# Kernel tuning notes

Measured on AMD Instinct MI355X. Metric: run time of the kernel, lower is better.

## Reference

```python
import jax, jax.numpy as jnp
import numpy as np

V_MIN = -10.0
V_MAX = 10.0
NUM_ATOMS = 251
B = 131072
N_OBS = 128
N_ACT = 32
HID = 512


def _ln(x, g, b, eps=1e-5):
    m = jnp.mean(x, axis=-1, keepdims=True)
    v = jnp.var(x, axis=-1, keepdims=True)
    return (x - m) * jax.lax.rsqrt(v + eps) * g + b


def setup_inputs() -> dict:
    key = jax.random.key(0)
    ks = jax.random.split(key, 16)

    def lin(k, fi, fo):
        kw, kb = jax.random.split(k)
        lim = 1.0 / np.sqrt(fi)
        W = jax.random.uniform(kw, (fi, fo), jnp.float32, -lim, lim)
        b = jax.random.uniform(kb, (fo,), jnp.float32, -lim, lim)
        return W, b

    W1, b1 = lin(ks[0], N_OBS + N_ACT, HID)
    W2, b2 = lin(ks[1], HID, HID // 2)
    W3, b3 = lin(ks[2], HID // 2, HID // 4)
    W4, b4 = lin(ks[3], HID // 4, NUM_ATOMS)

    return {
        "obs": jax.random.normal(ks[4], (B, N_OBS), jnp.float32),
        "actions": jax.random.normal(ks[5], (B, N_ACT), jnp.float32),
        "rewards": jax.random.normal(ks[6], (B,), jnp.float32),
        "bootstrap": (jax.random.uniform(ks[7], (B,)) > 0.05).astype(jnp.float32),
        "discount": jnp.full((B,), 0.99, jnp.float32),
        "q_support": jnp.linspace(V_MIN, V_MAX, NUM_ATOMS, dtype=jnp.float32),
        "W1": W1, "b1": b1, "g1": jnp.ones((HID,), jnp.float32), "be1": jnp.zeros((HID,), jnp.float32),
        "W2": W2, "b2": b2, "g2": jnp.ones((HID // 2,), jnp.float32), "be2": jnp.zeros((HID // 2,), jnp.float32),
        "W3": W3, "b3": b3, "g3": jnp.ones((HID // 4,), jnp.float32), "be3": jnp.zeros((HID // 4,), jnp.float32),
        "W4": W4, "b4": b4,
    }


def _net(obs, actions, W1, b1, g1, be1, W2, b2, g2, be2, W3, b3, g3, be3, W4, b4):
    x = jnp.concatenate([obs, actions], axis=1)
    x = jax.nn.silu(_ln(x @ W1 + b1, g1, be1))
    x = jax.nn.silu(_ln(x @ W2 + b2, g2, be2))
    x = jax.nn.silu(_ln(x @ W3 + b3, g3, be3))
    return x @ W4 + b4  # [B, NUM_ATOMS] logits


def reference(obs, actions, rewards, bootstrap, discount, q_support,
              W1, b1, g1, be1, W2, b2, g2, be2, W3, b3, g3, be3, W4, b4):
    # C51 categorical projection (DistributionalQNetwork.projection)
    delta_z = (V_MAX - V_MIN) / (NUM_ATOMS - 1)
    bsz = rewards.shape[0]
    target_z = rewards[:, None] + bootstrap[:, None] * discount[:, None] * q_support[None, :]
    target_z = jnp.clip(target_z, V_MIN, V_MAX)
    b = (target_z - V_MIN) / delta_z  # fractional bin positions [B, A]
    lower = jnp.floor(b).astype(jnp.int32)
    upper = jnp.ceil(b).astype(jnp.int32)
    is_integer = upper == lower
    lower_mask = (lower > 0) & is_integer
    upper_mask = (lower == 0) & is_integer
    lower = jnp.where(lower_mask, lower - 1, lower)
    upper = jnp.where(upper_mask, upper + 1, upper)

    logits = _net(obs, actions, W1, b1, g1, be1, W2, b2, g2, be2, W3, b3, g3, be3, W4, b4)
    next_dist = jax.nn.softmax(logits, axis=1)

    offset = (jnp.arange(bsz, dtype=jnp.int32) * NUM_ATOMS)[:, None]  # [B,1]
    max_index = bsz * NUM_ATOMS - 1
    li = jnp.clip((lower + offset).reshape(-1), 0, max_index)
    ui = jnp.clip((upper + offset).reshape(-1), 0, max_index)

    w_lo = (next_dist * (upper.astype(jnp.float32) - b)).reshape(-1)
    w_hi = (next_dist * (b - lower.astype(jnp.float32))).reshape(-1)

    proj = jnp.zeros((bsz * NUM_ATOMS,), next_dist.dtype)
    proj = proj.at[li].add(w_lo).at[ui].add(w_hi)
    return proj.reshape(bsz, NUM_ATOMS)
```

## Files before the change

kernel.cpp:

```cpp
#include <hip/hip_runtime.h>


#define THREADS 256
#define PREP_THREADS 256

typedef __attribute__((ext_vector_type(8))) short short8v;
typedef __attribute__((ext_vector_type(4))) float f32x4;

__device__ __forceinline__ unsigned short f2bf(float f) {
  union { float f; unsigned u; } v; v.f = f;
  unsigned u = v.u;
  u += 0x7fffu + ((u >> 16) & 1u);
  return (unsigned short)(u >> 16);
}
__device__ __forceinline__ unsigned pack2bf(float a, float b) {
  return (unsigned)f2bf(a) | ((unsigned)f2bf(b) << 16);
}

__global__ void prep_kernel(const float* __restrict__ W1, const float* __restrict__ W2,
                            const float* __restrict__ W3, const float* __restrict__ W4,
                            unsigned short* __restrict__ ws) {
  int i = blockIdx.x * PREP_THREADS + threadIdx.x;
  if (i < 81920) {
    int n = i / 160, k = i - n * 160;
    ws[i] = f2bf(W1[k * 512 + n]);
  } else if (i < 212992) {
    int j = i - 81920; int n = j >> 9, k = j & 511;
    ws[i] = f2bf(W2[k * 256 + n]);
  } else if (i < 245760) {
    int j = i - 212992; int n = j >> 8, k = j & 255;
    ws[i] = f2bf(W3[k * 128 + n]);
  } else if (i < 278528) {
    int j = i - 245760; int n = j >> 7, k = j & 127;
    ws[i] = (n < 251) ? f2bf(W4[k * 251 + n]) : (unsigned short)0;
  }
}

#define OFF_R   0
#define OFF_ZS  32768
#define OFF_B4  33792
#define OFF_RED 34816
#define LDS_TOTAL 36096

template<int KD, int NFT>
__device__ __forceinline__ void gemm_w(const unsigned short* __restrict__ WT,
                                       const unsigned char* __restrict__ Hb,
                                       int fbase, f32x4 (&acc)[NFT][2]) {
  const int lane = threadIdx.x & 63;
  const int lm = lane & 15, kg = lane >> 4;
  constexpr int KS  = KD / 32;
  constexpr int G   = (NFT > 4) ? 2 : 1;
  constexpr int FPG = NFT / G;
  constexpr int NIT = KS * G;

  int woff[NFT];
#pragma unroll
  for (int ft = 0; ft < NFT; ++ft)
    woff[ft] = (fbase + ft * 16 + lm) * KD + kg * 8;

  int boff[2][2];
#pragma unroll
  for (int rt = 0; rt < 2; ++rt) {
    const int r = rt * 16 + lm;
    const int swz = (r & 7) << 4;
    const int base = r * (KD * 2) + kg * 16;
    boff[rt][0] = base ^ swz;
    boff[rt][1] = (base + 64) ^ swz;
  }

  short8v abuf[2][FPG];
  short8v bbuf[2][2];
#pragma unroll
  for (int rt = 0; rt < 2; ++rt)
    bbuf[0][rt] = *(const short8v*)(Hb + boff[rt][0]);
#pragma unroll
  for (int f = 0; f < FPG; ++f)
    abuf[0][f] = *(const short8v*)(WT + woff[f]);

#pragma unroll
  for (int it = 0; it < NIT; ++it) {
    const int ks = it / G, g = it % G;
    const int cur = it & 1, nxt = cur ^ 1;
    if (it + 1 < NIT) {
      const int nit = it + 1;
      const int nks = nit / G, ng = nit % G;
      if (ng == 0) {
        const int koff = (nks >> 1) * 128;
#pragma unroll
        for (int rt = 0; rt < 2; ++rt)
          bbuf[nks & 1][rt] = *(const short8v*)(Hb + boff[rt][nks & 1] + koff);
      }
#pragma unroll
      for (int f = 0; f < FPG; ++f)
        abuf[nxt][f] = *(const short8v*)(WT + woff[ng * FPG + f] + nks * 32);
    }
#pragma unroll
    for (int f = 0; f < FPG; ++f) {
      const int ft = g * FPG + f;
      acc[ft][0] = __builtin_amdgcn_mfma_f32_16x16x32_bf16(abuf[cur][f], bbuf[ks & 1][0], acc[ft][0], 0, 0, 0);
      acc[ft][1] = __builtin_amdgcn_mfma_f32_16x16x32_bf16(abuf[cur][f], bbuf[ks & 1][1], acc[ft][1], 0, 0, 0);
    }
  }
}

template<int ND, int NFT>
__device__ __forceinline__ void ln_silu_store(
    f32x4 (&acc)[NFT][2],
    const float* __restrict__ bias, const float* __restrict__ g,
    const float* __restrict__ be, unsigned char* __restrict__ Hb,
    float* __restrict__ redL, int fbase, int fq)
{
  const int lane = threadIdx.x & 63;
  const int lm = lane & 15, kg = lane >> 4;
  float s[2] = {0.f, 0.f}, q[2] = {0.f, 0.f};
#pragma unroll
  for (int ft = 0; ft < NFT; ++ft) {
    const int f0 = fbase + ft * 16 + kg * 4;
    const f32x4 bb = *(const f32x4*)(bias + f0);
#pragma unroll
    for (int rt = 0; rt < 2; ++rt)
#pragma unroll
      for (int rg = 0; rg < 4; ++rg) {
        float x = acc[ft][rt][rg] + bb[rg];
        acc[ft][rt][rg] = x;
        s[rt] += x; q[rt] += x * x;
      }
  }
#pragma unroll
  for (int rt = 0; rt < 2; ++rt) {
    s[rt] += __shfl_xor(s[rt], 16); s[rt] += __shfl_xor(s[rt], 32);
    q[rt] += __shfl_xor(q[rt], 16); q[rt] += __shfl_xor(q[rt], 32);
  }
  if (lane < 16) {
#pragma unroll
    for (int rt = 0; rt < 2; ++rt) {
      redL[(rt * 16 + lm) * 9 + fq * 2    ] = s[rt];
      redL[(rt * 16 + lm) * 9 + fq * 2 + 1] = q[rt];
    }
  }
  __syncthreads();
  float mean[2], rstd[2];
#pragma unroll
  for (int rt = 0; rt < 2; ++rt) {
    const int row = rt * 16 + lm;
    float S = 0.f, Q = 0.f;
#pragma unroll
    for (int w = 0; w < 4; ++w) {
      S += redL[row * 9 + w * 2];
      Q += redL[row * 9 + w * 2 + 1];
    }
    float m = S * (1.0f / ND);
    float v = Q * (1.0f / ND) - m * m;
    mean[rt] = m; rstd[rt] = rsqrtf(v + 1e-5f);
  }
#pragma unroll
  for (int ft = 0; ft < NFT; ++ft) {
    const int f0 = fbase + ft * 16 + kg * 4;
    const f32x4 g4 = *(const f32x4*)(g + f0);
    const f32x4 e4 = *(const f32x4*)(be + f0);
#pragma unroll
    for (int rt = 0; rt < 2; ++rt) {
      const int row = rt * 16 + lm;
      float h[4];
#pragma unroll
      for (int rg = 0; rg < 4; ++rg) {
        float y = (acc[ft][rt][rg] - mean[rt]) * rstd[rt] * g4[rg] + e4[rg];
        h[rg] = y * (1.0f / (1.0f + __expf(-y)));
      }
      uint2 w; w.x = pack2bf(h[0], h[1]); w.y = pack2bf(h[2], h[3]);
      int byte = row * (ND * 2) + f0 * 2;
      byte ^= ((row & 7) << 4);
      *(uint2*)(Hb + byte) = w;
    }
  }
}

__global__ __launch_bounds__(THREADS, 4) void fused_kernel(
    const float* __restrict__ obs, const float* __restrict__ actions,
    const float* __restrict__ rewards, const float* __restrict__ bootstrap,
    const float* __restrict__ discount, const float* __restrict__ q_support,
    const float* __restrict__ b1, const float* __restrict__ g1, const float* __restrict__ be1,
    const float* __restrict__ b2, const float* __restrict__ g2, const float* __restrict__ be2,
    const float* __restrict__ b3, const float* __restrict__ g3, const float* __restrict__ be3,
    const float* __restrict__ b4,
    const unsigned short* __restrict__ ws,
    float* __restrict__ out)
{
  __shared__ __align__(16) unsigned char smem[LDS_TOTAL];
  const int tid  = threadIdx.x;
  const int fq   = tid >> 6;
  const int lane = tid & 63;
  const int lm   = lane & 15;
  const int kg   = lane >> 4;
  const int row0 = blockIdx.x * 32;

  const unsigned short* W1T = ws;
  const unsigned short* W2T = ws + 81920;
  const unsigned short* W3T = ws + 212992;
  const unsigned short* W4T = ws + 245760;

  float* zsL  = (float*)(smem + OFF_ZS);
  float* b4L  = (float*)(smem + OFF_B4);
  float* redL = (float*)(smem + OFF_RED);

  float rw[2], bt[2], dc[2];
#pragma unroll
  for (int rt = 0; rt < 2; ++rt) {
    const int r = row0 + rt * 16 + lm;
    rw[rt] = rewards[r]; bt[rt] = bootstrap[r]; dc[rt] = discount[r];
  }

  zsL[tid] = (tid < 251) ? q_support[tid] : 0.f;
  b4L[tid] = (tid < 251) ? b4[tid] : 0.f;

  {
    unsigned char* Xb = smem + OFF_R;
#pragma unroll
    for (int it = 0; it < 5; ++it) {
      const int qq = it * THREADS + tid;
      const int r  = qq / 40;
      const int c4 = (qq - r * 40) * 4;
      float4 v;
      if (c4 < 128) v = *(const float4*)(obs + (size_t)(row0 + r) * 128 + c4);
      else          v = *(const float4*)(actions + (size_t)(row0 + r) * 32 + (c4 - 128));
      uint2 w; w.x = pack2bf(v.x, v.y); w.y = pack2bf(v.z, v.w);
      int byte = r * 320 + c4 * 2;
      byte ^= ((r & 7) << 4);
      *(uint2*)(Xb + byte) = w;
    }
  }
  __syncthreads();

  f32x4 acc1[8][2];
#pragma unroll
  for (int i = 0; i < 8; ++i) { acc1[i][0] = f32x4{0,0,0,0}; acc1[i][1] = f32x4{0,0,0,0}; }
  gemm_w<160, 8>(W1T, smem + OFF_R, fq * 128, acc1);
  ln_silu_store<512, 8>(acc1, b1, g1, be1, smem + OFF_R, redL, fq * 128, fq);
  __syncthreads();

  f32x4 acc2[4][2];
#pragma unroll
  for (int i = 0; i < 4; ++i) { acc2[i][0] = f32x4{0,0,0,0}; acc2[i][1] = f32x4{0,0,0,0}; }
  gemm_w<512, 4>(W2T, smem + OFF_R, fq * 64, acc2);
  ln_silu_store<256, 4>(acc2, b2, g2, be2, smem + OFF_R, redL, fq * 64, fq);
  __syncthreads();

  f32x4 acc3[2][2];
#pragma unroll
  for (int i = 0; i < 2; ++i) { acc3[i][0] = f32x4{0,0,0,0}; acc3[i][1] = f32x4{0,0,0,0}; }
  gemm_w<256, 2>(W3T, smem + OFF_R, fq * 32, acc3);
  ln_silu_store<128, 2>(acc3, b3, g3, be3, smem + OFF_R, redL, fq * 32, fq);
  __syncthreads();

  f32x4 acc4[4][2];
#pragma unroll
  for (int i = 0; i < 4; ++i) { acc4[i][0] = f32x4{0,0,0,0}; acc4[i][1] = f32x4{0,0,0,0}; }
  gemm_w<128, 4>(W4T, smem + OFF_R, fq * 64, acc4);

  float lv[4][2][4];
#pragma unroll
  for (int ft = 0; ft < 4; ++ft) {
    const int f0 = fq * 64 + ft * 16 + kg * 4;
    const f32x4 bb = *(const f32x4*)(b4L + f0);
#pragma unroll
    for (int rt = 0; rt < 2; ++rt)
#pragma unroll
      for (int rg = 0; rg < 4; ++rg) {
        const int f = f0 + rg;
        lv[ft][rt][rg] = (f < 251) ? (acc4[ft][rt][rg] + bb[rg]) : -1e30f;
      }
  }

#pragma unroll
  for (int rt = 0; rt < 2; ++rt) {
    float m = lv[0][rt][0];
#pragma unroll
    for (int ft = 0; ft < 4; ++ft)
#pragma unroll
      for (int rg = 0; rg < 4; ++rg) m = fmaxf(m, lv[ft][rt][rg]);
    m = fmaxf(m, __shfl_xor(m, 16));
    m = fmaxf(m, __shfl_xor(m, 32));
    if (lane < 16) redL[(rt * 16 + lm) * 5 + fq] = m;
  }
  __syncthreads();

  float* projL = (float*)(smem + OFF_R);
  for (int i = tid; i < 32 * 251; i += THREADS) projL[i] = 0.f;

  float gm[2];
#pragma unroll
  for (int rt = 0; rt < 2; ++rt) {
    const int row = rt * 16 + lm;
    float m = redL[row * 5];
#pragma unroll
    for (int w = 1; w < 4; ++w) m = fmaxf(m, redL[row * 5 + w]);
    gm[rt] = m;
  }
  __syncthreads();
#pragma unroll
  for (int rt = 0; rt < 2; ++rt) {
    float E = 0.f;
#pragma unroll
    for (int ft = 0; ft < 4; ++ft)
#pragma unroll
      for (int rg = 0; rg < 4; ++rg) {
        float e = __expf(lv[ft][rt][rg] - gm[rt]);
        lv[ft][rt][rg] = e;
        E += e;
      }
    E += __shfl_xor(E, 16); E += __shfl_xor(E, 32);
    if (lane < 16) redL[(rt * 16 + lm) * 5 + fq] = E;
  }
  __syncthreads();
  float inv[2];
#pragma unroll
  for (int rt = 0; rt < 2; ++rt) {
    const int row = rt * 16 + lm;
    float E = 0.f;
#pragma unroll
    for (int w = 0; w < 4; ++w) E += redL[row * 5 + w];
    inv[rt] = 1.0f / E;
  }

  constexpr float DZF = 20.0f / 250.0f;
#pragma unroll
  for (int ft = 0; ft < 4; ++ft) {
    const int f0 = fq * 64 + ft * 16 + kg * 4;
    const f32x4 z4 = *(const f32x4*)(zsL + f0);
#pragma unroll
    for (int rt = 0; rt < 2; ++rt) {
      const int base = (rt * 16 + lm) * 251;
      const float bd = __fmul_rn(bt[rt], dc[rt]);
#pragma unroll
      for (int rg = 0; rg < 4; ++rg) {
        const int f = f0 + rg;
        if (f < 251) {
          const float p = lv[ft][rt][rg] * inv[rt];
          float t = __fadd_rn(rw[rt], __fmul_rn(bd, z4[rg]));
          t = fminf(fmaxf(t, -10.0f), 10.0f);
          const float bfr = __fdiv_rn(__fsub_rn(t, -10.0f), DZF);
          const float fl = floorf(bfr), fu = ceilf(bfr);
          int l = (int)fl, u = (int)fu;
          if (fl == fu) { if (l > 0) --l; else ++u; }
          atomicAdd(projL + base + l, p * ((float)u - bfr));
          atomicAdd(projL + base + u, p * (bfr - (float)l));
        }
      }
    }
  }
  __syncthreads();

  const float4* ps = (const float4*)projL;
  float4* po = (float4*)(out + (size_t)row0 * 251);
  for (int i = tid; i < 2008; i += THREADS) po[i] = ps[i];
}

extern "C" void kernel_launch(void* const* d_in, const int* in_sizes, int n_in,
                              void* d_out, int out_size, void* d_ws, size_t ws_size,
                              hipStream_t stream) {
  const float* obs  = (const float*)d_in[0];
  const float* act  = (const float*)d_in[1];
  const float* rew  = (const float*)d_in[2];
  const float* boot = (const float*)d_in[3];
  const float* disc = (const float*)d_in[4];
  const float* zs   = (const float*)d_in[5];
  const float* W1   = (const float*)d_in[6];
  const float* b1   = (const float*)d_in[7];
  const float* g1   = (const float*)d_in[8];
  const float* be1  = (const float*)d_in[9];
  const float* W2   = (const float*)d_in[10];
  const float* b2   = (const float*)d_in[11];
  const float* g2   = (const float*)d_in[12];
  const float* be2  = (const float*)d_in[13];
  const float* W3   = (const float*)d_in[14];
  const float* b3   = (const float*)d_in[15];
  const float* g3   = (const float*)d_in[16];
  const float* be3  = (const float*)d_in[17];
  const float* W4   = (const float*)d_in[18];
  const float* b4   = (const float*)d_in[19];
  unsigned short* wsp = (unsigned short*)d_ws;

  const int Bn = in_sizes[2];
  prep_kernel<<<(278528 + PREP_THREADS - 1) / PREP_THREADS, PREP_THREADS, 0, stream>>>(
      W1, W2, W3, W4, wsp);
  fused_kernel<<<Bn / 32, THREADS, 0, stream>>>(obs, act, rew, boot, disc, zs,
      b1, g1, be1, b2, g2, be2, b3, g3, be3, b4, wsp, (float*)d_out);
}
```

Baseline: 482.8 us.

## Halve rows per block to 16 and use hardware bf16 pack instruction

Each block now handles 16 batch rows instead of 32, so every MFMA uses one B tile rather than two. This halves accumulator registers and LDS, and the launch bound rises to 6 blocks per SM for higher occupancy. It also replaces the software bf16 rounding in pack2bf with the v_cvt_pk_bf16_f32 instruction. The cost is that each weight fragment loaded from global or L2 is reused across half as many rows, which doubles weight traffic per row.

```diff
diff --git a/kernel.cpp b/kernel.cpp
--- a/kernel.cpp
+++ b/kernel.cpp
@@ -14,7 +14,9 @@
   return (unsigned short)(u >> 16);
 }
 __device__ __forceinline__ unsigned pack2bf(float a, float b) {
-  return (unsigned)f2bf(a) | ((unsigned)f2bf(b) << 16);
+  unsigned r;
+  asm("v_cvt_pk_bf16_f32 %0, %1, %2" : "=v"(r) : "v"(a), "v"(b));
+  return r;
 }
 
 __global__ void prep_kernel(const float* __restrict__ W1, const float* __restrict__ W2,
@@ -37,15 +39,15 @@
 }
 
 #define OFF_R   0
-#define OFF_ZS  32768
-#define OFF_B4  33792
-#define OFF_RED 34816
-#define LDS_TOTAL 36096
+#define OFF_ZS  16384
+#define OFF_B4  17408
+#define OFF_RED 18432
+#define LDS_TOTAL 19008
 
 template<int KD, int NFT>
 __device__ __forceinline__ void gemm_w(const unsigned short* __restrict__ WT,
                                        const unsigned char* __restrict__ Hb,
-                                       int fbase, f32x4 (&acc)[NFT][2]) {
+                                       int fbase, f32x4 (&acc)[NFT]) {
   const int lane = threadIdx.x & 63;
   const int lm = lane & 15, kg = lane >> 4;
   constexpr int KS  = KD / 32;
@@ -53,29 +55,19 @@
   constexpr int FPG = NFT / G;
   constexpr int NIT = KS * G;
 
-  int woff[NFT];
-#pragma unroll
-  for (int ft = 0; ft < NFT; ++ft)
-    woff[ft] = (fbase + ft * 16 + lm) * KD + kg * 8;
-
-  int boff[2][2];
-#pragma unroll
-  for (int rt = 0; rt < 2; ++rt) {
-    const int r = rt * 16 + lm;
-    const int swz = (r & 7) << 4;
-    const int base = r * (KD * 2) + kg * 16;
-    boff[rt][0] = base ^ swz;
-    boff[rt][1] = (base + 64) ^ swz;
-  }
+  const int woff0 = (fbase + lm) * KD + kg * 8;
+  const int r = lm;
+  const int swz = (r & 7) << 4;
+  const int bbase = r * (KD * 2) + kg * 16;
+  const int boff0 = bbase ^ swz;
+  const int boff1 = (bbase + 64) ^ swz;
 
   short8v abuf[2][FPG];
-  short8v bbuf[2][2];
-#pragma unroll
-  for (int rt = 0; rt < 2; ++rt)
-    bbuf[0][rt] = *(const short8v*)(Hb + boff[rt][0]);
+  short8v bbuf[2];
+  bbuf[0] = *(const short8v*)(Hb + boff0);
 #pragma unroll
   for (int f = 0; f < FPG; ++f)
-    abuf[0][f] = *(const short8v*)(WT + woff[f]);
+    abuf[0][f] = *(const short8v*)(WT + woff0 + f * (16 * KD));
 
 #pragma unroll
   for (int it = 0; it < NIT; ++it) {
@@ -86,96 +78,76 @@
       const int nks = nit / G, ng = nit % G;
       if (ng == 0) {
         const int koff = (nks >> 1) * 128;
-#pragma unroll
-        for (int rt = 0; rt < 2; ++rt)
-          bbuf[nks & 1][rt] = *(const short8v*)(Hb + boff[rt][nks & 1] + koff);
+        bbuf[nks & 1] = *(const short8v*)(Hb + ((nks & 1) ? boff1 : boff0) + koff);
       }
 #pragma unroll
       for (int f = 0; f < FPG; ++f)
-        abuf[nxt][f] = *(const short8v*)(WT + woff[ng * FPG + f] + nks * 32);
+        abuf[nxt][f] = *(const short8v*)(WT + woff0 + (ng * FPG + f) * (16 * KD) + nks * 32);
     }
 #pragma unroll
     for (int f = 0; f < FPG; ++f) {
       const int ft = g * FPG + f;
-      acc[ft][0] = __builtin_amdgcn_mfma_f32_16x16x32_bf16(abuf[cur][f], bbuf[ks & 1][0], acc[ft][0], 0, 0, 0);
-      acc[ft][1] = __builtin_amdgcn_mfma_f32_16x16x32_bf16(abuf[cur][f], bbuf[ks & 1][1], acc[ft][1], 0, 0, 0);
+      acc[ft] = __builtin_amdgcn_mfma_f32_16x16x32_bf16(abuf[cur][f], bbuf[ks & 1], acc[ft], 0, 0, 0);
     }
   }
 }
 
 template<int ND, int NFT>
 __device__ __forceinline__ void ln_silu_store(
-    f32x4 (&acc)[NFT][2],
+    f32x4 (&acc)[NFT],
     const float* __restrict__ bias, const float* __restrict__ g,
     const float* __restrict__ be, unsigned char* __restrict__ Hb,
     float* __restrict__ redL, int fbase, int fq)
 {
   const int lane = threadIdx.x & 63;
   const int lm = lane & 15, kg = lane >> 4;
-  float s[2] = {0.f, 0.f}, q[2] = {0.f, 0.f};
+  float s = 0.f, q = 0.f;
 #pragma unroll
   for (int ft = 0; ft < NFT; ++ft) {
     const int f0 = fbase + ft * 16 + kg * 4;
     const f32x4 bb = *(const f32x4*)(bias + f0);
 #pragma unroll
-    for (int rt = 0; rt < 2; ++rt)
-#pragma unroll
-      for (int rg = 0; rg < 4; ++rg) {
-        float x = acc[ft][rt][rg] + bb[rg];
-        acc[ft][rt][rg] = x;
-        s[rt] += x; q[rt] += x * x;
-      }
-  }
-#pragma unroll
-  for (int rt = 0; rt < 2; ++rt) {
-    s[rt] += __shfl_xor(s[rt], 16); s[rt] += __shfl_xor(s[rt], 32);
-    q[rt] += __shfl_xor(q[rt], 16); q[rt] += __shfl_xor(q[rt], 32);
-  }
+    for (int rg = 0; rg < 4; ++rg) {
+      float x = acc[ft][rg] + bb[rg];
+      acc[ft][rg] = x;
+      s += x; q += x * x;
+    }
+  }
+  s += __shfl_xor(s, 16); s += __shfl_xor(s, 32);
+  q += __shfl_xor(q, 16); q += __shfl_xor(q, 32);
   if (lane < 16) {
-#pragma unroll
-    for (int rt = 0; rt < 2; ++rt) {
-      redL[(rt * 16 + lm) * 9 + fq * 2    ] = s[rt];
-      redL[(rt * 16 + lm) * 9 + fq * 2 + 1] = q[rt];
-    }
-  }
-  __syncthreads();
-  float mean[2], rstd[2];
-#pragma unroll
-  for (int rt = 0; rt < 2; ++rt) {
-    const int row = rt * 16 + lm;
-    float S = 0.f, Q = 0.f;
-#pragma unroll
-    for (int w = 0; w < 4; ++w) {
-      S += redL[row * 9 + w * 2];
-      Q += redL[row * 9 + w * 2 + 1];
-    }
-    float m = S * (1.0f / ND);
-    float v = Q * (1.0f / ND) - m * m;
-    mean[rt] = m; rstd[rt] = rsqrtf(v + 1e-5f);
-  }
+    redL[lm * 9 + fq * 2    ] = s;
+    redL[lm * 9 + fq * 2 + 1] = q;
+  }
+  __syncthreads();
+  float S = 0.f, Q = 0.f;
+#pragma unroll
+  for (int w = 0; w < 4; ++w) {
+    S += redL[lm * 9 + w * 2];
+    Q += redL[lm * 9 + w * 2 + 1];
+  }
+  const float mean = S * (1.0f / ND);
+  const float var  = Q * (1.0f / ND) - mean * mean;
+  const float rstd = rsqrtf(var + 1e-5f);
 #pragma unroll
   for (int ft = 0; ft < NFT; ++ft) {
     const int f0 = fbase + ft * 16 + kg * 4;
     const f32x4 g4 = *(const f32x4*)(g + f0);
     const f32x4 e4 = *(const f32x4*)(be + f0);
-#pragma unroll
-    for (int rt = 0; rt < 2; ++rt) {
-      const int row = rt * 16 + lm;
-      float h[4];
-#pragma unroll
-      for (int rg = 0; rg < 4; ++rg) {
-        float y = (acc[ft][rt][rg] - mean[rt]) * rstd[rt] * g4[rg] + e4[rg];
-        h[rg] = y * (1.0f / (1.0f + __expf(-y)));
-      }
-      uint2 w; w.x = pack2bf(h[0], h[1]); w.y = pack2bf(h[2], h[3]);
-      int byte = row * (ND * 2) + f0 * 2;
-      byte ^= ((row & 7) << 4);
-      *(uint2*)(Hb + byte) = w;
-    }
-  }
-}
-
-__global__ __launch_bounds__(THREADS, 4) void fused_kernel(
+    float h[4];
+#pragma unroll
+    for (int rg = 0; rg < 4; ++rg) {
+      float y = (acc[ft][rg] - mean) * rstd * g4[rg] + e4[rg];
+      h[rg] = y * (1.0f / (1.0f + __expf(-y)));
+    }
+    uint2 w; w.x = pack2bf(h[0], h[1]); w.y = pack2bf(h[2], h[3]);
+    int byte = lm * (ND * 2) + f0 * 2;
+    byte ^= ((lm & 7) << 4);
+    *(uint2*)(Hb + byte) = w;
+  }
+}
+
+__global__ __launch_bounds__(THREADS, 6) void fused_kernel(
     const float* __restrict__ obs, const float* __restrict__ actions,
     const float* __restrict__ rewards, const float* __restrict__ bootstrap,
     const float* __restrict__ discount, const float* __restrict__ q_support,
@@ -192,7 +164,7 @@
   const int lane = tid & 63;
   const int lm   = lane & 15;
   const int kg   = lane >> 4;
-  const int row0 = blockIdx.x * 32;
+  const int row0 = blockIdx.x * 16;
 
   const unsigned short* W1T = ws;
   const unsigned short* W2T = ws + 81920;
@@ -203,21 +175,17 @@
   float* b4L  = (float*)(smem + OFF_B4);
   float* redL = (float*)(smem + OFF_RED);
 
-  float rw[2], bt[2], dc[2];
-#pragma unroll
-  for (int rt = 0; rt < 2; ++rt) {
-    const int r = row0 + rt * 16 + lm;
-    rw[rt] = rewards[r]; bt[rt] = bootstrap[r]; dc[rt] = discount[r];
-  }
+  const int rr = row0 + lm;
+  const float rw = rewards[rr];
+  const float bt = bootstrap[rr];
+  const float dc = discount[rr];
 
   zsL[tid] = (tid < 251) ? q_support[tid] : 0.f;
   b4L[tid] = (tid < 251) ? b4[tid] : 0.f;
 
   {
     unsigned char* Xb = smem + OFF_R;
-#pragma unroll
-    for (int it = 0; it < 5; ++it) {
-      const int qq = it * THREADS + tid;
+    for (int qq = tid; qq < 640; qq += THREADS) {
       const int r  = qq / 40;
       const int c4 = (qq - r * 40) * 4;
       float4 v;
@@ -231,120 +199,109 @@
   }
   __syncthreads();
 
-  f32x4 acc1[8][2];
-#pragma unroll
-  for (int i = 0; i < 8; ++i) { acc1[i][0] = f32x4{0,0,0,0}; acc1[i][1] = f32x4{0,0,0,0}; }
+  f32x4 acc1[8];
+#pragma unroll
+  for (int i = 0; i < 8; ++i) acc1[i] = f32x4{0.f, 0.f, 0.f, 0.f};
   gemm_w<160, 8>(W1T, smem + OFF_R, fq * 128, acc1);
   ln_silu_store<512, 8>(acc1, b1, g1, be1, smem + OFF_R, redL, fq * 128, fq);
   __syncthreads();
 
-  f32x4 acc2[4][2];
-#pragma unroll
-  for (int i = 0; i < 4; ++i) { acc2[i][0] = f32x4{0,0,0,0}; acc2[i][1] = f32x4{0,0,0,0}; }
+  f32x4 acc2[4];
+#pragma unroll
+  for (int i = 0; i < 4; ++i) acc2[i] = f32x4{0.f, 0.f, 0.f, 0.f};
   gemm_w<512, 4>(W2T, smem + OFF_R, fq * 64, acc2);
   ln_silu_store<256, 4>(acc2, b2, g2, be2, smem + OFF_R, redL, fq * 64, fq);
   __syncthreads();
 
-  f32x4 acc3[2][2];
-#pragma unroll
-  for (int i = 0; i < 2; ++i) { acc3[i][0] = f32x4{0,0,0,0}; acc3[i][1] = f32x4{0,0,0,0}; }
+  f32x4 acc3[2];
+  acc3[0] = f32x4{0.f, 0.f, 0.f, 0.f};
+  acc3[1] = f32x4{0.f, 0.f, 0.f, 0.f};
   gemm_w<256, 2>(W3T, smem + OFF_R, fq * 32, acc3);
   ln_silu_store<128, 2>(acc3, b3, g3, be3, smem + OFF_R, redL, fq * 32, fq);
   __syncthreads();
 
-  f32x4 acc4[4][2];
-#pragma unroll
-  for (int i = 0; i < 4; ++i) { acc4[i][0] = f32x4{0,0,0,0}; acc4[i][1] = f32x4{0,0,0,0}; }
+  f32x4 acc4[4];
+#pragma unroll
+  for (int i = 0; i < 4; ++i) acc4[i] = f32x4{0.f, 0.f, 0.f, 0.f};
   gemm_w<128, 4>(W4T, smem + OFF_R, fq * 64, acc4);
 
-  float lv[4][2][4];
+  float lv[4][4];
 #pragma unroll
   for (int ft = 0; ft < 4; ++ft) {
     const int f0 = fq * 64 + ft * 16 + kg * 4;
     const f32x4 bb = *(const f32x4*)(b4L + f0);
 #pragma unroll
-    for (int rt = 0; rt < 2; ++rt)
-#pragma unroll
-      for (int rg = 0; rg < 4; ++rg) {
-        const int f = f0 + rg;
-        lv[ft][rt][rg] = (f < 251) ? (acc4[ft][rt][rg] + bb[rg]) : -1e30f;
-      }
-  }
-
-#pragma unroll
-  for (int rt = 0; rt < 2; ++rt) {
-    float m = lv[0][rt][0];
+    for (int rg = 0; rg < 4; ++rg) {
+      const int f = f0 + rg;
+      lv[ft][rg] = (f < 251) ? (acc4[ft][rg] + bb[rg]) : -1e30f;
+    }
+  }
+
+  {
+    float m = lv[0][0];
 #pragma unroll
     for (int ft = 0; ft < 4; ++ft)
 #pragma unroll
-      for (int rg = 0; rg < 4; ++rg) m = fmaxf(m, lv[ft][rt][rg]);
+      for (int rg = 0; rg < 4; ++rg) m = fmaxf(m, lv[ft][rg]);
     m = fmaxf(m, __shfl_xor(m, 16));
     m = fmaxf(m, __shfl_xor(m, 32));
-    if (lane < 16) redL[(rt * 16 + lm) * 5 + fq] = m;
+    if (lane < 16) redL[lm * 5 + fq] = m;
   }
   __syncthreads();
 
   float* projL = (float*)(smem + OFF_R);
-  for (int i = tid; i < 32 * 251; i += THREADS) projL[i] = 0.f;
-
-  float gm[2];
-#pragma unroll
-  for (int rt = 0; rt < 2; ++rt) {
-    const int row = rt * 16 + lm;
-    float m = redL[row * 5];
-#pragma unroll
-    for (int w = 1; w < 4; ++w) m = fmaxf(m, redL[row * 5 + w]);
-    gm[rt] = m;
-  }
-  __syncthreads();
-#pragma unroll
-  for (int rt = 0; rt < 2; ++rt) {
+  for (int i = tid; i < 16 * 251; i += THREADS) projL[i] = 0.f;
+
+  float gm;
+  {
+    float m = redL[lm * 5];
+#pragma unroll
+    for (int w = 1; w < 4; ++w) m = fmaxf(m, redL[lm * 5 + w]);
+    gm = m;
+  }
+  __syncthreads();
+  {
     float E = 0.f;
 #pragma unroll
     for (int ft = 0; ft < 4; ++ft)
 #pragma unroll
       for (int rg = 0; rg < 4; ++rg) {
-        float e = __expf(lv[ft][rt][rg] - gm[rt]);
-        lv[ft][rt][rg] = e;
+        float e = __expf(lv[ft][rg] - gm);
+        lv[ft][rg] = e;
         E += e;
       }
     E += __shfl_xor(E, 16); E += __shfl_xor(E, 32);
-    if (lane < 16) redL[(rt * 16 + lm) * 5 + fq] = E;
-  }
-  __syncthreads();
-  float inv[2];
-#pragma unroll
-  for (int rt = 0; rt < 2; ++rt) {
-    const int row = rt * 16 + lm;
+    if (lane < 16) redL[lm * 5 + fq] = E;
+  }
+  __syncthreads();
+  float inv;
+  {
     float E = 0.f;
 #pragma unroll
-    for (int w = 0; w < 4; ++w) E += redL[row * 5 + w];
-    inv[rt] = 1.0f / E;
+    for (int w = 0; w < 4; ++w) E += redL[lm * 5 + w];
+    inv = 1.0f / E;
   }
 
   constexpr float DZF = 20.0f / 250.0f;
+  const int base = lm * 251;
+  const float bd = __fmul_rn(bt, dc);
 #pragma unroll
   for (int ft = 0; ft < 4; ++ft) {
     const int f0 = fq * 64 + ft * 16 + kg * 4;
     const f32x4 z4 = *(const f32x4*)(zsL + f0);
 #pragma unroll
-    for (int rt = 0; rt < 2; ++rt) {
-      const int base = (rt * 16 + lm) * 251;
-      const float bd = __fmul_rn(bt[rt], dc[rt]);
-#pragma unroll
-      for (int rg = 0; rg < 4; ++rg) {
-        const int f = f0 + rg;
-        if (f < 251) {
-          const float p = lv[ft][rt][rg] * inv[rt];
-          float t = __fadd_rn(rw[rt], __fmul_rn(bd, z4[rg]));
-          t = fminf(fmaxf(t, -10.0f), 10.0f);
-          const float bfr = __fdiv_rn(__fsub_rn(t, -10.0f), DZF);
-          const float fl = floorf(bfr), fu = ceilf(bfr);
-          int l = (int)fl, u = (int)fu;
-          if (fl == fu) { if (l > 0) --l; else ++u; }
-          atomicAdd(projL + base + l, p * ((float)u - bfr));
-          atomicAdd(projL + base + u, p * (bfr - (float)l));
-        }
+    for (int rg = 0; rg < 4; ++rg) {
+      const int f = f0 + rg;
+      if (f < 251) {
+        const float p = lv[ft][rg] * inv;
+        float t = __fadd_rn(rw, __fmul_rn(bd, z4[rg]));
+        t = fminf(fmaxf(t, -10.0f), 10.0f);
+        const float bfr = __fdiv_rn(__fsub_rn(t, -10.0f), DZF);
+        const float fl = floorf(bfr), fu = ceilf(bfr);
+        int l = (int)fl, u = (int)fu;
+        if (fl == fu) { if (l > 0) --l; else ++u; }
+        atomicAdd(projL + base + l, p * ((float)u - bfr));
+        atomicAdd(projL + base + u, p * (bfr - (float)l));
       }
     }
   }
@@ -352,7 +309,7 @@
 
   const float4* ps = (const float4*)projL;
   float4* po = (float4*)(out + (size_t)row0 * 251);
-  for (int i = tid; i < 2008; i += THREADS) po[i] = ps[i];
+  for (int i = tid; i < 1004; i += THREADS) po[i] = ps[i];
 }
 
 extern "C" void kernel_launch(void* const* d_in, const int* in_sizes, int n_in,
@@ -383,6 +340,6 @@
   const int Bn = in_sizes[2];
   prep_kernel<<<(278528 + PREP_THREADS - 1) / PREP_THREADS, PREP_THREADS, 0, stream>>>(
       W1, W2, W3, W4, wsp);
-  fused_kernel<<<Bn / 32, THREADS, 0, stream>>>(obs, act, rew, boot, disc, zs,
+  fused_kernel<<<Bn / 16, THREADS, 0, stream>>>(obs, act, rew, boot, disc, zs,
       b1, g1, be1, b2, g2, be2, b3, g3, be3, b4, wsp, (float*)d_out);
 }
```

Result: slower. 554.3 us (+14.8%).
